# Kernel optimization log

Hardware: AMD Instinct MI355X
Metric: run time of the kernel (lower is better)

Reference implementation:

```python
import jax, jax.numpy as jnp
import numpy as np

B, S, D, V = 64, 128, 64, 50000

def _prelu(x, a):
    return jnp.where(x >= 0, x, a * x)

def setup_inputs() -> dict:
    key = jax.random.key(0)
    ks = jax.random.split(key, 24)
    stdv = 1.0 / np.sqrt(D)
    u = lambda k, shape: jax.random.uniform(k, shape, jnp.float32, -stdv, stdv)
    emb = u(ks[0], (V, D)).at[0].set(0.0)  # padding_idx=0
    inp = {
        'items': jax.random.randint(ks[1], (B, S), 0, V),
        'A': jax.random.randint(ks[2], (B, S, S), 0, 2),
        'edgeorder': jax.random.randint(ks[3], (B, S, S), 0, S),
        'last_nodes': jax.random.randint(ks[4], (B,), 0, S),
        'mask': jnp.ones((B, S), dtype=bool),
        'emb': emb,
        'W_self': u(ks[5], (D, D)), 'W_neigh': u(ks[6], (D, D)),
        'prelu1': jnp.full((D,), 0.25, jnp.float32),
        'Wq': u(ks[7], (D, D)), 'bq': jnp.zeros((D,), jnp.float32),
        'Wk': u(ks[8], (D, D)), 'Wv': u(ks[9], (D, D)), 'we': u(ks[10], (D,)),
        'prelu2': jnp.full((D,), 0.25, jnp.float32),
        'Wu': u(ks[11], (D, D)), 'bu': jnp.zeros((D,), jnp.float32),
        'Wvr': u(ks[12], (D, D)), 'wer': u(ks[13], (D,)),
        'prelu3': jnp.full((D,), 0.25, jnp.float32),
        'W_sr': u(ks[14], (2 * D, D)),
    }
    return inp

def reference(items, A, edgeorder, last_nodes, mask, emb, W_self, W_neigh, prelu1,
              Wq, bq, Wk, Wv, we, prelu2, Wu, bu, Wvr, wer, prelu3, W_sr):
    x = emb[items]  # [B,S,D]
    # ---- EOPA: masked neighbor broadcast + edgeorder gather + max-pool ----
    adjT = (jnp.swapaxes(A, 1, 2) == 1)  # [B,S(target),S(neighbor)]
    neigh = jnp.where((adjT & mask[:, None, :])[..., None], x[:, None, :, :], 0.0)  # [B,S,S,D]
    eo_t = jnp.swapaxes(edgeorder, 1, 2)  # [B,S,S]
    # gathered[b,i,j,:] = neigh[b, edgeorder[b,j,i], j, :]
    neigh = jnp.take_along_axis(neigh, eo_t[..., None], axis=1)
    neigh = neigh.max(axis=2)  # [B,S,D]
    h = _prelu(x @ W_self + neigh @ W_neigh, prelu1)
    # ---- SGAT: sigmoid-gated attention over adjacency ----
    q = h @ Wq + bq
    k = h @ Wk
    v = h @ Wv
    e = k[:, :, None, :] + q[:, None, :, :]             # e[b,i,j,d]
    e = jnp.where((A == 1)[..., None], e, 0.0)
    e = jax.nn.sigmoid(e) @ we                           # [B,S,S]
    a = jax.nn.softmax(e, axis=1)                        # softmax over source i
    h2 = _prelu(jnp.einsum('bij,bid->bjd', a, v), prelu2)
    # ---- AttnReadout ----
    xu = h2 @ Wu + bu                                    # [B,S,D]
    xlast = h2[jnp.arange(h2.shape[0]), last_nodes]      # [B,D]
    xv = xlast @ Wvr
    eatt = jax.nn.sigmoid(xu + xv[:, None, :]) @ wer     # [B,S]
    alpha = jax.nn.softmax(eatt, axis=1)
    out = _prelu((h2 * alpha[..., None]).sum(axis=1), prelu3)  # [B,D]
    # ---- session representation ----
    sr = jnp.concatenate([out, xlast], axis=-1) @ W_sr   # [B,D]
    return sr
```

## Files before the change

kernel.cpp:

```cpp
#include <hip/hip_runtime.h>

#define BB 64
#define SS 128
#define DD 64
#define SSQ (SS*SS)
#define BSD (BB*SS*DD)

__device__ __forceinline__ float fast_sigmoid(float x) {
  return __builtin_amdgcn_rcpf(1.0f + __expf(-x));
}

__global__ __launch_bounds__(256) void k12_eopa_hqkv(
    const int* __restrict__ items, const int* __restrict__ Aadj,
    const int* __restrict__ eo, const float* __restrict__ emb,
    const float* __restrict__ Wself, const float* __restrict__ Wneigh,
    const float* __restrict__ prelu1,
    const float* __restrict__ Wq, const float* __restrict__ bq,
    const float* __restrict__ Wk, const float* __restrict__ Wv,
    float* __restrict__ q_ws, float* __restrict__ k_ws, float* __restrict__ v_ws)
{
  __shared__ alignas(16) float xs[SS*DD];
  __shared__ alignas(16) float nms[32*DD];
  __shared__ alignas(16) float Wb[DD*DD];
  __shared__ unsigned int condw[SS];
  float* hs = nms;

  const int b  = blockIdx.x >> 2;
  const int iq = blockIdx.x & 3;
  const int tid = threadIdx.x;
  const int wv = tid >> 6, lane = tid & 63;
  const int d = lane;

  const float4* emb4 = (const float4*)emb;
  float4* xs4 = (float4*)xs;
  for (int f = tid; f < SS*16; f += 256) {
    int j = f >> 4, qd = f & 15;
    xs4[f] = emb4[items[b*SS + j]*16 + qd];
  }
  {
    const float4* W4 = (const float4*)Wself; float4* Wb4 = (float4*)Wb;
    for (int f = tid; f < 1024; f += 256) Wb4[f] = W4[f];
  }
  {
    int eov[16];
#pragma unroll
    for (int k = 0; k < 16; k++) {
      int p = tid + k*256;
      eov[k] = eo[b*SSQ + (p >> 5)*SS + iq*32 + (p & 31)];
    }
#pragma unroll
    for (int k = 0; k < 16; k++) {
      int p = tid + k*256;
      bool c = (Aadj[b*SSQ + (p >> 5)*SS + eov[k]] == 1);
      unsigned long long bm = __ballot(c);
      if (lane == 0) {
        int j0 = ((tid & ~63) + k*256) >> 5;
        condw[j0]     = (unsigned int)bm;
        condw[j0 + 1] = (unsigned int)(bm >> 32);
      }
    }
  }
  __syncthreads();

  {
    float m[8];
#pragma unroll
    for (int r = 0; r < 8; r++) m[r] = -__builtin_inff();
    for (int j = 0; j < SS; j++) {
      unsigned int cw = condw[j] >> (wv*8);
      float xv = xs[j*DD + d];
#pragma unroll
      for (int r = 0; r < 8; r++) {
        float val = ((cw >> r) & 1u) ? xv : 0.0f;
        m[r] = fmaxf(m[r], val);
      }
    }
#pragma unroll
    for (int r = 0; r < 8; r++) nms[(wv*8 + r)*DD + d] = m[r];
  }

  float acc[8];
#pragma unroll
  for (int t = 0; t < 8; t++) acc[t] = 0.0f;
  for (int kk = 0; kk < DD; kk++) {
    float w = Wb[kk*DD + d];
#pragma unroll
    for (int t = 0; t < 8; t++)
      acc[t] = fmaf(xs[(iq*32 + wv*8 + t)*DD + kk], w, acc[t]);
  }
  __syncthreads();
  {
    const float4* W4 = (const float4*)Wneigh; float4* Wb4 = (float4*)Wb;
    for (int f = tid; f < 1024; f += 256) Wb4[f] = W4[f];
  }
  __syncthreads();
  for (int kk = 0; kk < DD; kk++) {
    float w = Wb[kk*DD + d];
#pragma unroll
    for (int t = 0; t < 8; t++)
      acc[t] = fmaf(nms[(wv*8 + t)*DD + kk], w, acc[t]);
  }
  float h2r[8];
  {
    float p1 = prelu1[d];
#pragma unroll
    for (int t = 0; t < 8; t++) {
      float h = acc[t];
      h2r[t] = (h >= 0.0f) ? h : p1*h;
    }
  }
  __syncthreads();
#pragma unroll
  for (int t = 0; t < 8; t++) hs[(wv*8 + t)*DD + d] = h2r[t];
  {
    const float4* W4 = (const float4*)Wq; float4* Wb4 = (float4*)Wb;
    for (int f = tid; f < 1024; f += 256) Wb4[f] = W4[f];
  }
  __syncthreads();
  const int r0g = b*SS + iq*32;
  {
    float bqv = bq[d];
#pragma unroll
    for (int t = 0; t < 8; t++) acc[t] = bqv;
    for (int kk = 0; kk < DD; kk++) {
      float w = Wb[kk*DD + d];
#pragma unroll
      for (int t = 0; t < 8; t++) acc[t] = fmaf(hs[(wv*8 + t)*DD + kk], w, acc[t]);
    }
#pragma unroll
    for (int t = 0; t < 8; t++) q_ws[(r0g + wv*8 + t)*DD + d] = acc[t];
  }
  __syncthreads();
  {
    const float4* W4 = (const float4*)Wk; float4* Wb4 = (float4*)Wb;
    for (int f = tid; f < 1024; f += 256) Wb4[f] = W4[f];
  }
  __syncthreads();
  {
#pragma unroll
    for (int t = 0; t < 8; t++) acc[t] = 0.0f;
    for (int kk = 0; kk < DD; kk++) {
      float w = Wb[kk*DD + d];
#pragma unroll
      for (int t = 0; t < 8; t++) acc[t] = fmaf(hs[(wv*8 + t)*DD + kk], w, acc[t]);
    }
#pragma unroll
    for (int t = 0; t < 8; t++) k_ws[(r0g + wv*8 + t)*DD + d] = acc[t];
  }
  __syncthreads();
  {
    const float4* W4 = (const float4*)Wv; float4* Wb4 = (float4*)Wb;
    for (int f = tid; f < 1024; f += 256) Wb4[f] = W4[f];
  }
  __syncthreads();
  {
#pragma unroll
    for (int t = 0; t < 8; t++) acc[t] = 0.0f;
    for (int kk = 0; kk < DD; kk++) {
      float w = Wb[kk*DD + d];
#pragma unroll
      for (int t = 0; t < 8; t++) acc[t] = fmaf(hs[(wv*8 + t)*DD + kk], w, acc[t]);
    }
#pragma unroll
    for (int t = 0; t < 8; t++) v_ws[(r0g + wv*8 + t)*DD + d] = acc[t];
  }
}

__global__ __launch_bounds__(256) void k3_sgat(
    const int* __restrict__ Aadj,
    const float* __restrict__ q_ws, const float* __restrict__ k_ws,
    const float* __restrict__ v_ws,
    const float* __restrict__ we, const float* __restrict__ prelu2,
    const float* __restrict__ Wu, const float* __restrict__ bu,
    float* __restrict__ h2_ws, float* __restrict__ xu_ws)
{
  __shared__ float ks[SS*65];
  __shared__ alignas(16) float pool[32*SS + 32*DD];
  __shared__ float wes[DD];
  float* es = pool;
  float* qs = pool + 32*SS;
  const int b  = blockIdx.x >> 2;
  const int j0 = (blockIdx.x & 3) * 32;
  const int tid = threadIdx.x;
  const int wv = tid >> 6, lane = tid & 63;

  for (int f = tid; f < SS*DD; f += 256) {
    int i = f >> 6, d = f & 63;
    ks[i*65 + d] = k_ws[(b*SS + i)*DD + d];
  }
  for (int f = tid; f < 32*DD; f += 256)
    qs[f] = q_ws[(b*SS + j0)*DD + f];
  if (tid < DD) wes[tid] = we[tid];
  float hw = we[lane];
  for (int off = 32; off >= 1; off >>= 1) hw += __shfl_xor(hw, off);
  const float half_sum = 0.5f * hw;
  __syncthreads();

  for (int p = tid; p < 32*SS; p += 256) {
    int i  = p & (SS-1);
    int jl = p >> 7;
    float e2;
    if (Aadj[b*SSQ + i*SS + j0 + jl] == 1) {
      float s = 0.0f;
      for (int d2 = 0; d2 < DD; d2++) {
        float t = ks[i*65 + d2] + qs[jl*DD + d2];
        s = fmaf(wes[d2], fast_sigmoid(t), s);
      }
      e2 = s;
    } else {
      e2 = half_sum;
    }
    es[jl*SS + i] = e2;
  }
  __syncthreads();

  float* vs = ks;
  for (int f = tid; f < SS*DD; f += 256)
    vs[f] = v_ws[b*SS*DD + f];
  for (int t = 0; t < 8; t++) {
    int jl = wv*8 + t;
    float a0 = es[jl*SS + lane], a1 = es[jl*SS + 64 + lane];
    float mx = fmaxf(a0, a1);
    for (int off = 32; off >= 1; off >>= 1) mx = fmaxf(mx, __shfl_xor(mx, off));
    float p0 = __expf(a0 - mx), p1 = __expf(a1 - mx);
    float sm = p0 + p1;
    for (int off = 32; off >= 1; off >>= 1) sm += __shfl_xor(sm, off);
    float inv = 1.0f / sm;
    es[jl*SS + lane]      = p0 * inv;
    es[jl*SS + 64 + lane] = p1 * inv;
  }
  __syncthreads();

  float acc[8];
#pragma unroll
  for (int t = 0; t < 8; t++) acc[t] = 0.0f;
  for (int i = 0; i < SS; i++) {
    float vv = vs[i*DD + lane];
#pragma unroll
    for (int t = 0; t < 8; t++) acc[t] = fmaf(es[(wv*8+t)*SS + i], vv, acc[t]);
  }
  float h2r[8];
  {
    float p2 = prelu2[lane];
#pragma unroll
    for (int t = 0; t < 8; t++) {
      float h2 = acc[t];
      h2r[t] = (h2 >= 0.0f) ? h2 : p2*h2;
      h2_ws[(b*SS + j0 + wv*8 + t)*DD + lane] = h2r[t];
    }
  }
  __syncthreads();

  float* hs2 = pool;
  float* Wus = pool + 32*DD;
#pragma unroll
  for (int t = 0; t < 8; t++) hs2[(wv*8+t)*DD + lane] = h2r[t];
  {
    const float4* W4 = (const float4*)Wu; float4* Wus4 = (float4*)Wus;
    for (int f = tid; f < 1024; f += 256) Wus4[f] = W4[f];
  }
  __syncthreads();
  {
    float buv = bu[lane];
    float acc2[8];
#pragma unroll
    for (int t = 0; t < 8; t++) acc2[t] = buv;
    for (int kk = 0; kk < DD; kk++) {
      float w = Wus[kk*DD + lane];
#pragma unroll
      for (int t = 0; t < 8; t++) acc2[t] = fmaf(hs2[(wv*8+t)*DD + kk], w, acc2[t]);
    }
#pragma unroll
    for (int t = 0; t < 8; t++)
      xu_ws[(b*SS + j0 + wv*8 + t)*DD + lane] = acc2[t];
  }
}

__global__ __launch_bounds__(256) void k4_readout(
    const float* __restrict__ h2_ws, const float* __restrict__ xu_ws,
    const int* __restrict__ last_nodes,
    const float* __restrict__ Wvr, const float* __restrict__ wer,
    const float* __restrict__ prelu3, const float* __restrict__ Wsr,
    float* __restrict__ out)
{
  __shared__ float xlast[DD], xv[DD], eatt[SS], alpha[SS], outs[DD];
  __shared__ float pools[4*DD];
  const int b = blockIdx.x;
  const int tid = threadIdx.x;
  const int wv = tid >> 6, lane = tid & 63;

  const int ln = last_nodes[b];
  if (tid < DD) xlast[tid] = h2_ws[(b*SS + ln)*DD + tid];
  __syncthreads();
  if (tid < DD) {
    float s = 0.0f;
    for (int k2 = 0; k2 < DD; k2++)
      s = fmaf(xlast[k2], Wvr[k2*DD + tid], s);
    xv[tid] = s;
  }
  __syncthreads();
  {
    float werv = wer[lane];
    float xvl = xv[lane];
    for (int j = wv; j < SS; j += 4) {
      float xuv = xu_ws[(b*SS + j)*DD + lane];
      float term = fast_sigmoid(xuv + xvl) * werv;
      for (int off = 32; off >= 1; off >>= 1) term += __shfl_xor(term, off);
      if (lane == 0) eatt[j] = term;
    }
  }
  __syncthreads();
  if (wv == 0) {
    float a0 = eatt[lane], a1 = eatt[64 + lane];
    float mx = fmaxf(a0, a1);
    for (int off = 32; off >= 1; off >>= 1) mx = fmaxf(mx, __shfl_xor(mx, off));
    float p0 = __expf(a0 - mx), p1 = __expf(a1 - mx);
    float sm = p0 + p1;
    for (int off = 32; off >= 1; off >>= 1) sm += __shfl_xor(sm, off);
    float inv = 1.0f / sm;
    alpha[lane]      = p0 * inv;
    alpha[64 + lane] = p1 * inv;
  }
  __syncthreads();
  {
    float part = 0.0f;
    for (int j = wv; j < SS; j += 4)
      part = fmaf(alpha[j], h2_ws[(b*SS + j)*DD + lane], part);
    pools[wv*DD + lane] = part;
  }
  __syncthreads();
  if (wv == 0) {
    float s = pools[lane] + pools[DD + lane] + pools[2*DD + lane] + pools[3*DD + lane];
    float p3 = prelu3[lane];
    outs[lane] = (s >= 0.0f) ? s : p3 * s;
  }
  __syncthreads();
  {
    float fs = 0.0f;
    for (int m2 = wv*32; m2 < wv*32 + 32; m2++) {
      float src = (m2 < DD) ? outs[m2] : xlast[m2 - DD];
      fs = fmaf(src, Wsr[m2*DD + lane], fs);
    }
    pools[wv*DD + lane] = fs;
  }
  __syncthreads();
  if (wv == 0)
    out[b*DD + lane] = pools[lane] + pools[DD + lane] + pools[2*DD + lane] + pools[3*DD + lane];
}

extern "C" void kernel_launch(void* const* d_in, const int* in_sizes, int n_in,
                              void* d_out, int out_size, void* d_ws, size_t ws_size,
                              hipStream_t stream)
{
  const int* items = (const int*)d_in[0];
  const int* Aadj  = (const int*)d_in[1];
  const int* eo    = (const int*)d_in[2];
  const int* lastn = (const int*)d_in[3];
  const float* emb    = (const float*)d_in[5];
  const float* Wself  = (const float*)d_in[6];
  const float* Wneigh = (const float*)d_in[7];
  const float* p1     = (const float*)d_in[8];
  const float* Wq     = (const float*)d_in[9];
  const float* bq     = (const float*)d_in[10];
  const float* Wk     = (const float*)d_in[11];
  const float* Wv     = (const float*)d_in[12];
  const float* we     = (const float*)d_in[13];
  const float* p2     = (const float*)d_in[14];
  const float* Wu     = (const float*)d_in[15];
  const float* bu     = (const float*)d_in[16];
  const float* Wvr    = (const float*)d_in[17];
  const float* wer    = (const float*)d_in[18];
  const float* p3     = (const float*)d_in[19];
  const float* Wsr    = (const float*)d_in[20];

  float* ws    = (float*)d_ws;
  float* q_ws  = ws;
  float* k_ws  = ws + (size_t)BSD;
  float* v_ws  = ws + (size_t)2*BSD;
  float* h2_ws = ws + (size_t)3*BSD;
  float* xu_ws = ws + (size_t)4*BSD;

  k12_eopa_hqkv<<<BB*4, 256, 0, stream>>>(items, Aadj, eo, emb, Wself, Wneigh, p1,
                                          Wq, bq, Wk, Wv, q_ws, k_ws, v_ws);
  k3_sgat<<<BB*4, 256, 0, stream>>>(Aadj, q_ws, k_ws, v_ws, we, p2, Wu, bu,
                                    h2_ws, xu_ws);
  k4_readout<<<BB, 256, 0, stream>>>(h2_ws, xu_ws, lastn, Wvr, wer, p3, Wsr,
                                     (float*)d_out);
}
```

Baseline: 204.0 us.

## Double grid size to 16-row tiles, double-buffer weights, vectorize loads

Splits each batch across 8 blocks of 16 rows instead of 4 blocks of 32 in the EOPA/QKV and SGAT kernels, so 512 blocks fill more compute units on the GPU. It double-buffers weight matrices in shared memory so the next weight loads overlap the current matmul and removes some barriers. It also pads the q/es tiles, uses float4 loads for k/v, and widens the readout kernel to 512 threads. The cost is that each block redundantly reloads the full embedding and K/V tiles, which doubles that global traffic.

```diff
diff --git a/kernel.cpp b/kernel.cpp
--- a/kernel.cpp
+++ b/kernel.cpp
@@ -10,7 +10,7 @@
   return __builtin_amdgcn_rcpf(1.0f + __expf(-x));
 }
 
-__global__ __launch_bounds__(256) void k12_eopa_hqkv(
+__global__ __launch_bounds__(256) void kA(
     const int* __restrict__ items, const int* __restrict__ Aadj,
     const int* __restrict__ eo, const float* __restrict__ emb,
     const float* __restrict__ Wself, const float* __restrict__ Wneigh,
@@ -20,153 +20,152 @@
     float* __restrict__ q_ws, float* __restrict__ k_ws, float* __restrict__ v_ws)
 {
   __shared__ alignas(16) float xs[SS*DD];
-  __shared__ alignas(16) float nms[32*DD];
-  __shared__ alignas(16) float Wb[DD*DD];
-  __shared__ unsigned int condw[SS];
-  float* hs = nms;
-
-  const int b  = blockIdx.x >> 2;
-  const int iq = blockIdx.x & 3;
+  __shared__ alignas(16) float Wb[2][DD*DD];
+  __shared__ alignas(16) float nms[16*DD];
+  __shared__ alignas(16) float hs[16*DD];
+  __shared__ unsigned short condw[SS];
+  const int b  = blockIdx.x >> 3;
+  const int i0 = (blockIdx.x & 7) * 16;
   const int tid = threadIdx.x;
   const int wv = tid >> 6, lane = tid & 63;
-  const int d = lane;
-
-  const float4* emb4 = (const float4*)emb;
-  float4* xs4 = (float4*)xs;
-  for (int f = tid; f < SS*16; f += 256) {
-    int j = f >> 4, qd = f & 15;
-    xs4[f] = emb4[items[b*SS + j]*16 + qd];
-  }
-  {
-    const float4* W4 = (const float4*)Wself; float4* Wb4 = (float4*)Wb;
+
+  {
+    const float4* emb4 = (const float4*)emb;
+    float4* xs4 = (float4*)xs;
+    for (int f = tid; f < SS*16; f += 256) {
+      int j = f >> 4, qd = f & 15;
+      xs4[f] = emb4[items[b*SS + j]*16 + qd];
+    }
+    const float4* W4 = (const float4*)Wself;
+    float4* Wb4 = (float4*)Wb[0];
     for (int f = tid; f < 1024; f += 256) Wb4[f] = W4[f];
   }
   {
-    int eov[16];
-#pragma unroll
-    for (int k = 0; k < 16; k++) {
+    int eov[8];
+#pragma unroll
+    for (int k = 0; k < 8; k++) {
       int p = tid + k*256;
-      eov[k] = eo[b*SSQ + (p >> 5)*SS + iq*32 + (p & 31)];
-    }
-#pragma unroll
-    for (int k = 0; k < 16; k++) {
+      eov[k] = eo[b*SSQ + (p >> 4)*SS + i0 + (p & 15)];
+    }
+#pragma unroll
+    for (int k = 0; k < 8; k++) {
       int p = tid + k*256;
-      bool c = (Aadj[b*SSQ + (p >> 5)*SS + eov[k]] == 1);
+      bool c = (Aadj[b*SSQ + (p >> 4)*SS + eov[k]] == 1);
       unsigned long long bm = __ballot(c);
-      if (lane == 0) {
-        int j0 = ((tid & ~63) + k*256) >> 5;
-        condw[j0]     = (unsigned int)bm;
-        condw[j0 + 1] = (unsigned int)(bm >> 32);
+      if ((lane & 15) == 0)
+        condw[p >> 4] = (unsigned short)(bm >> lane);
+    }
+  }
+  __syncthreads();
+
+  {
+    const float4* W4 = (const float4*)Wneigh;
+    float4* Wb4 = (float4*)Wb[1];
+    for (int f = tid; f < 1024; f += 256) Wb4[f] = W4[f];
+  }
+  {
+    float m[4];
+#pragma unroll
+    for (int t = 0; t < 4; t++) m[t] = -__builtin_inff();
+    for (int j = 0; j < SS; j++) {
+      unsigned int cw = (unsigned int)condw[j] >> (wv*4);
+      float xv = xs[j*DD + lane];
+#pragma unroll
+      for (int t = 0; t < 4; t++) {
+        float val = ((cw >> t) & 1u) ? xv : 0.0f;
+        m[t] = fmaxf(m[t], val);
       }
     }
-  }
-  __syncthreads();
-
-  {
-    float m[8];
-#pragma unroll
-    for (int r = 0; r < 8; r++) m[r] = -__builtin_inff();
-    for (int j = 0; j < SS; j++) {
-      unsigned int cw = condw[j] >> (wv*8);
-      float xv = xs[j*DD + d];
-#pragma unroll
-      for (int r = 0; r < 8; r++) {
-        float val = ((cw >> r) & 1u) ? xv : 0.0f;
-        m[r] = fmaxf(m[r], val);
-      }
-    }
-#pragma unroll
-    for (int r = 0; r < 8; r++) nms[(wv*8 + r)*DD + d] = m[r];
-  }
-
-  float acc[8];
-#pragma unroll
-  for (int t = 0; t < 8; t++) acc[t] = 0.0f;
+#pragma unroll
+    for (int t = 0; t < 4; t++) nms[(wv*4 + t)*DD + lane] = m[t];
+  }
+  float acc[4];
+#pragma unroll
+  for (int t = 0; t < 4; t++) acc[t] = 0.0f;
   for (int kk = 0; kk < DD; kk++) {
-    float w = Wb[kk*DD + d];
-#pragma unroll
-    for (int t = 0; t < 8; t++)
-      acc[t] = fmaf(xs[(iq*32 + wv*8 + t)*DD + kk], w, acc[t]);
-  }
-  __syncthreads();
-  {
-    const float4* W4 = (const float4*)Wneigh; float4* Wb4 = (float4*)Wb;
+    float w = Wb[0][kk*DD + lane];
+#pragma unroll
+    for (int t = 0; t < 4; t++)
+      acc[t] = fmaf(xs[(i0 + wv*4 + t)*DD + kk], w, acc[t]);
+  }
+  __syncthreads();
+
+  {
+    const float4* W4 = (const float4*)Wq;
+    float4* Wb4 = (float4*)Wb[0];
     for (int f = tid; f < 1024; f += 256) Wb4[f] = W4[f];
   }
-  __syncthreads();
   for (int kk = 0; kk < DD; kk++) {
-    float w = Wb[kk*DD + d];
-#pragma unroll
-    for (int t = 0; t < 8; t++)
-      acc[t] = fmaf(nms[(wv*8 + t)*DD + kk], w, acc[t]);
-  }
-  float h2r[8];
-  {
-    float p1 = prelu1[d];
-#pragma unroll
-    for (int t = 0; t < 8; t++) {
+    float w = Wb[1][kk*DD + lane];
+#pragma unroll
+    for (int t = 0; t < 4; t++)
+      acc[t] = fmaf(nms[(wv*4 + t)*DD + kk], w, acc[t]);
+  }
+  {
+    float p1 = prelu1[lane];
+#pragma unroll
+    for (int t = 0; t < 4; t++) {
       float h = acc[t];
-      h2r[t] = (h >= 0.0f) ? h : p1*h;
-    }
-  }
-  __syncthreads();
-#pragma unroll
-  for (int t = 0; t < 8; t++) hs[(wv*8 + t)*DD + d] = h2r[t];
-  {
-    const float4* W4 = (const float4*)Wq; float4* Wb4 = (float4*)Wb;
+      hs[(wv*4 + t)*DD + lane] = (h >= 0.0f) ? h : p1*h;
+    }
+  }
+  __syncthreads();
+
+  const int r0g = b*SS + i0;
+  {
+    const float4* W4 = (const float4*)Wk;
+    float4* Wb4 = (float4*)Wb[1];
     for (int f = tid; f < 1024; f += 256) Wb4[f] = W4[f];
   }
-  __syncthreads();
-  const int r0g = b*SS + iq*32;
-  {
-    float bqv = bq[d];
-#pragma unroll
-    for (int t = 0; t < 8; t++) acc[t] = bqv;
+  {
+    float bqv = bq[lane];
+#pragma unroll
+    for (int t = 0; t < 4; t++) acc[t] = bqv;
     for (int kk = 0; kk < DD; kk++) {
-      float w = Wb[kk*DD + d];
-#pragma unroll
-      for (int t = 0; t < 8; t++) acc[t] = fmaf(hs[(wv*8 + t)*DD + kk], w, acc[t]);
-    }
-#pragma unroll
-    for (int t = 0; t < 8; t++) q_ws[(r0g + wv*8 + t)*DD + d] = acc[t];
-  }
-  __syncthreads();
-  {
-    const float4* W4 = (const float4*)Wk; float4* Wb4 = (float4*)Wb;
+      float w = Wb[0][kk*DD + lane];
+#pragma unroll
+      for (int t = 0; t < 4; t++)
+        acc[t] = fmaf(hs[(wv*4 + t)*DD + kk], w, acc[t]);
+    }
+#pragma unroll
+    for (int t = 0; t < 4; t++) q_ws[(r0g + wv*4 + t)*DD + lane] = acc[t];
+  }
+  __syncthreads();
+
+  {
+    const float4* W4 = (const float4*)Wv;
+    float4* Wb4 = (float4*)Wb[0];
     for (int f = tid; f < 1024; f += 256) Wb4[f] = W4[f];
   }
-  __syncthreads();
-  {
-#pragma unroll
-    for (int t = 0; t < 8; t++) acc[t] = 0.0f;
+  {
+#pragma unroll
+    for (int t = 0; t < 4; t++) acc[t] = 0.0f;
     for (int kk = 0; kk < DD; kk++) {
-      float w = Wb[kk*DD + d];
-#pragma unroll
-      for (int t = 0; t < 8; t++) acc[t] = fmaf(hs[(wv*8 + t)*DD + kk], w, acc[t]);
-    }
-#pragma unroll
-    for (int t = 0; t < 8; t++) k_ws[(r0g + wv*8 + t)*DD + d] = acc[t];
-  }
-  __syncthreads();
-  {
-    const float4* W4 = (const float4*)Wv; float4* Wb4 = (float4*)Wb;
-    for (int f = tid; f < 1024; f += 256) Wb4[f] = W4[f];
-  }
-  __syncthreads();
-  {
-#pragma unroll
-    for (int t = 0; t < 8; t++) acc[t] = 0.0f;
+      float w = Wb[1][kk*DD + lane];
+#pragma unroll
+      for (int t = 0; t < 4; t++)
+        acc[t] = fmaf(hs[(wv*4 + t)*DD + kk], w, acc[t]);
+    }
+#pragma unroll
+    for (int t = 0; t < 4; t++) k_ws[(r0g + wv*4 + t)*DD + lane] = acc[t];
+  }
+  __syncthreads();
+
+  {
+#pragma unroll
+    for (int t = 0; t < 4; t++) acc[t] = 0.0f;
     for (int kk = 0; kk < DD; kk++) {
-      float w = Wb[kk*DD + d];
-#pragma unroll
-      for (int t = 0; t < 8; t++) acc[t] = fmaf(hs[(wv*8 + t)*DD + kk], w, acc[t]);
-    }
-#pragma unroll
-    for (int t = 0; t < 8; t++) v_ws[(r0g + wv*8 + t)*DD + d] = acc[t];
+      float w = Wb[0][kk*DD + lane];
+#pragma unroll
+      for (int t = 0; t < 4; t++)
+        acc[t] = fmaf(hs[(wv*4 + t)*DD + kk], w, acc[t]);
+    }
+#pragma unroll
+    for (int t = 0; t < 4; t++) v_ws[(r0g + wv*4 + t)*DD + lane] = acc[t];
   }
 }
 
-__global__ __launch_bounds__(256) void k3_sgat(
+__global__ __launch_bounds__(256) void kB(
     const int* __restrict__ Aadj,
     const float* __restrict__ q_ws, const float* __restrict__ k_ws,
     const float* __restrict__ v_ws,
@@ -174,109 +173,127 @@
     const float* __restrict__ Wu, const float* __restrict__ bu,
     float* __restrict__ h2_ws, float* __restrict__ xu_ws)
 {
-  __shared__ float ks[SS*65];
-  __shared__ alignas(16) float pool[32*SS + 32*DD];
+  __shared__ alignas(16) float ks[SS*65];
+  __shared__ alignas(16) float qs[16*65];
+  __shared__ alignas(16) float es[16*129];
   __shared__ float wes[DD];
-  float* es = pool;
-  float* qs = pool + 32*SS;
-  const int b  = blockIdx.x >> 2;
-  const int j0 = (blockIdx.x & 3) * 32;
+  const int b  = blockIdx.x >> 3;
+  const int j0 = (blockIdx.x & 7) * 16;
   const int tid = threadIdx.x;
   const int wv = tid >> 6, lane = tid & 63;
 
-  for (int f = tid; f < SS*DD; f += 256) {
-    int i = f >> 6, d = f & 63;
-    ks[i*65 + d] = k_ws[(b*SS + i)*DD + d];
-  }
-  for (int f = tid; f < 32*DD; f += 256)
-    qs[f] = q_ws[(b*SS + j0)*DD + f];
+  {
+    const float4* k4 = (const float4*)k_ws;
+    for (int f = tid; f < 2048; f += 256) {
+      int i = f >> 4, d4 = f & 15;
+      float4 v = k4[(b*SS + i)*16 + d4];
+      float* dst = &ks[i*65 + d4*4];
+      dst[0] = v.x; dst[1] = v.y; dst[2] = v.z; dst[3] = v.w;
+    }
+    const float4* q4 = (const float4*)q_ws;
+    for (int f = tid; f < 256; f += 256) {
+      int jl = f >> 4, d4 = f & 15;
+      float4 v = q4[(b*SS + j0 + jl)*16 + d4];
+      float* dst = &qs[jl*65 + d4*4];
+      dst[0] = v.x; dst[1] = v.y; dst[2] = v.z; dst[3] = v.w;
+    }
+  }
   if (tid < DD) wes[tid] = we[tid];
   float hw = we[lane];
   for (int off = 32; off >= 1; off >>= 1) hw += __shfl_xor(hw, off);
   const float half_sum = 0.5f * hw;
   __syncthreads();
 
-  for (int p = tid; p < 32*SS; p += 256) {
-    int i  = p & (SS-1);
-    int jl = p >> 7;
+#pragma unroll
+  for (int k = 0; k < 8; k++) {
+    int p = tid + k*256;
+    int jl = p & 15, i = p >> 4;
     float e2;
     if (Aadj[b*SSQ + i*SS + j0 + jl] == 1) {
       float s = 0.0f;
       for (int d2 = 0; d2 < DD; d2++) {
-        float t = ks[i*65 + d2] + qs[jl*DD + d2];
+        float t = ks[i*65 + d2] + qs[jl*65 + d2];
         s = fmaf(wes[d2], fast_sigmoid(t), s);
       }
       e2 = s;
     } else {
       e2 = half_sum;
     }
-    es[jl*SS + i] = e2;
+    es[jl*129 + i] = e2;
   }
   __syncthreads();
 
   float* vs = ks;
-  for (int f = tid; f < SS*DD; f += 256)
-    vs[f] = v_ws[b*SS*DD + f];
-  for (int t = 0; t < 8; t++) {
-    int jl = wv*8 + t;
-    float a0 = es[jl*SS + lane], a1 = es[jl*SS + 64 + lane];
+  {
+    const float4* v4 = (const float4*)v_ws;
+    float4* vs4 = (float4*)vs;
+    for (int f = tid; f < 2048; f += 256)
+      vs4[f] = v4[b*SS*16 + f];
+  }
+#pragma unroll
+  for (int t = 0; t < 4; t++) {
+    int jl = wv*4 + t;
+    float a0 = es[jl*129 + lane], a1 = es[jl*129 + 64 + lane];
     float mx = fmaxf(a0, a1);
     for (int off = 32; off >= 1; off >>= 1) mx = fmaxf(mx, __shfl_xor(mx, off));
     float p0 = __expf(a0 - mx), p1 = __expf(a1 - mx);
     float sm = p0 + p1;
     for (int off = 32; off >= 1; off >>= 1) sm += __shfl_xor(sm, off);
     float inv = 1.0f / sm;
-    es[jl*SS + lane]      = p0 * inv;
-    es[jl*SS + 64 + lane] = p1 * inv;
-  }
-  __syncthreads();
-
-  float acc[8];
-#pragma unroll
-  for (int t = 0; t < 8; t++) acc[t] = 0.0f;
+    es[jl*129 + lane]      = p0 * inv;
+    es[jl*129 + 64 + lane] = p1 * inv;
+  }
+  __syncthreads();
+
+  float acc[4];
+#pragma unroll
+  for (int t = 0; t < 4; t++) acc[t] = 0.0f;
   for (int i = 0; i < SS; i++) {
     float vv = vs[i*DD + lane];
 #pragma unroll
-    for (int t = 0; t < 8; t++) acc[t] = fmaf(es[(wv*8+t)*SS + i], vv, acc[t]);
-  }
-  float h2r[8];
+    for (int t = 0; t < 4; t++)
+      acc[t] = fmaf(es[(wv*4 + t)*129 + i], vv, acc[t]);
+  }
+  float h2r[4];
   {
     float p2 = prelu2[lane];
 #pragma unroll
-    for (int t = 0; t < 8; t++) {
+    for (int t = 0; t < 4; t++) {
       float h2 = acc[t];
       h2r[t] = (h2 >= 0.0f) ? h2 : p2*h2;
-      h2_ws[(b*SS + j0 + wv*8 + t)*DD + lane] = h2r[t];
-    }
-  }
-  __syncthreads();
-
-  float* hs2 = pool;
-  float* Wus = pool + 32*DD;
-#pragma unroll
-  for (int t = 0; t < 8; t++) hs2[(wv*8+t)*DD + lane] = h2r[t];
-  {
-    const float4* W4 = (const float4*)Wu; float4* Wus4 = (float4*)Wus;
+      h2_ws[(b*SS + j0 + wv*4 + t)*DD + lane] = h2r[t];
+    }
+  }
+  __syncthreads();
+
+  float* hs2 = es;
+  float* Wus = ks;
+#pragma unroll
+  for (int t = 0; t < 4; t++) hs2[(wv*4 + t)*DD + lane] = h2r[t];
+  {
+    const float4* W4 = (const float4*)Wu;
+    float4* Wus4 = (float4*)Wus;
     for (int f = tid; f < 1024; f += 256) Wus4[f] = W4[f];
   }
   __syncthreads();
   {
     float buv = bu[lane];
-    float acc2[8];
-#pragma unroll
-    for (int t = 0; t < 8; t++) acc2[t] = buv;
+    float acc2[4];
+#pragma unroll
+    for (int t = 0; t < 4; t++) acc2[t] = buv;
     for (int kk = 0; kk < DD; kk++) {
       float w = Wus[kk*DD + lane];
 #pragma unroll
-      for (int t = 0; t < 8; t++) acc2[t] = fmaf(hs2[(wv*8+t)*DD + kk], w, acc2[t]);
-    }
-#pragma unroll
-    for (int t = 0; t < 8; t++)
-      xu_ws[(b*SS + j0 + wv*8 + t)*DD + lane] = acc2[t];
+      for (int t = 0; t < 4; t++)
+        acc2[t] = fmaf(hs2[(wv*4 + t)*DD + kk], w, acc2[t]);
+    }
+#pragma unroll
+    for (int t = 0; t < 4; t++)
+      xu_ws[(b*SS + j0 + wv*4 + t)*DD + lane] = acc2[t];
   }
 }
 
-__global__ __launch_bounds__(256) void k4_readout(
+__global__ __launch_bounds__(512) void k4_readout(
     const float* __restrict__ h2_ws, const float* __restrict__ xu_ws,
     const int* __restrict__ last_nodes,
     const float* __restrict__ Wvr, const float* __restrict__ wer,
@@ -284,7 +301,7 @@
     float* __restrict__ out)
 {
   __shared__ float xlast[DD], xv[DD], eatt[SS], alpha[SS], outs[DD];
-  __shared__ float pools[4*DD];
+  __shared__ float pools[8*DD];
   const int b = blockIdx.x;
   const int tid = threadIdx.x;
   const int wv = tid >> 6, lane = tid & 63;
@@ -302,7 +319,7 @@
   {
     float werv = wer[lane];
     float xvl = xv[lane];
-    for (int j = wv; j < SS; j += 4) {
+    for (int j = wv; j < SS; j += 8) {
       float xuv = xu_ws[(b*SS + j)*DD + lane];
       float term = fast_sigmoid(xuv + xvl) * werv;
       for (int off = 32; off >= 1; off >>= 1) term += __shfl_xor(term, off);
@@ -324,28 +341,34 @@
   __syncthreads();
   {
     float part = 0.0f;
-    for (int j = wv; j < SS; j += 4)
+    for (int j = wv; j < SS; j += 8)
       part = fmaf(alpha[j], h2_ws[(b*SS + j)*DD + lane], part);
     pools[wv*DD + lane] = part;
   }
   __syncthreads();
   if (wv == 0) {
-    float s = pools[lane] + pools[DD + lane] + pools[2*DD + lane] + pools[3*DD + lane];
+    float s = 0.0f;
+#pragma unroll
+    for (int w = 0; w < 8; w++) s += pools[w*DD + lane];
     float p3 = prelu3[lane];
     outs[lane] = (s >= 0.0f) ? s : p3 * s;
   }
   __syncthreads();
   {
     float fs = 0.0f;
-    for (int m2 = wv*32; m2 < wv*32 + 32; m2++) {
+    for (int m2 = wv*16; m2 < wv*16 + 16; m2++) {
       float src = (m2 < DD) ? outs[m2] : xlast[m2 - DD];
       fs = fmaf(src, Wsr[m2*DD + lane], fs);
     }
     pools[wv*DD + lane] = fs;
   }
   __syncthreads();
-  if (wv == 0)
-    out[b*DD + lane] = pools[lane] + pools[DD + lane] + pools[2*DD + lane] + pools[3*DD + lane];
+  if (wv == 0) {
+    float s = 0.0f;
+#pragma unroll
+    for (int w = 0; w < 8; w++) s += pools[w*DD + lane];
+    out[b*DD + lane] = s;
+  }
 }
 
 extern "C" void kernel_launch(void* const* d_in, const int* in_sizes, int n_in,
@@ -380,10 +403,10 @@
   float* h2_ws = ws + (size_t)3*BSD;
   float* xu_ws = ws + (size_t)4*BSD;
 
-  k12_eopa_hqkv<<<BB*4, 256, 0, stream>>>(items, Aadj, eo, emb, Wself, Wneigh, p1,
-                                          Wq, bq, Wk, Wv, q_ws, k_ws, v_ws);
-  k3_sgat<<<BB*4, 256, 0, stream>>>(Aadj, q_ws, k_ws, v_ws, we, p2, Wu, bu,
-                                    h2_ws, xu_ws);
-  k4_readout<<<BB, 256, 0, stream>>>(h2_ws, xu_ws, lastn, Wvr, wer, p3, Wsr,
+  kA<<<BB*8, 256, 0, stream>>>(items, Aadj, eo, emb, Wself, Wneigh, p1,
+                               Wq, bq, Wk, Wv, q_ws, k_ws, v_ws);
+  kB<<<BB*8, 256, 0, stream>>>(Aadj, q_ws, k_ws, v_ws, we, p2, Wu, bu,
+                               h2_ws, xu_ws);
+  k4_readout<<<BB, 512, 0, stream>>>(h2_ws, xu_ws, lastn, Wvr, wer, p3, Wsr,
                                      (float*)d_out);
 }
```

Measured after the change: 183.8 us. -9.9%, faster.
